# Kernel tuning notes

Hardware: AMD Instinct MI355X
Metric: run time of the kernel (lower is better)

## Reference

```python
import jax, jax.numpy as jnp
import numpy as np

D_MODEL = 512; DEPTH = 4; HEADS = 8; BUCKET = 256; N_HASHES = 4
INPUT_DIM = 32; SEQ = 2 * BUCKET; BATCH = 16; DH = D_MODEL // HEADS
N_BUCKETS = SEQ // BUCKET  # 2 (seq_len is forced to 2*bucket_size by pos_encoding)
SELF_ATTN_VALUE = -5e4  # TOKEN_SELF_ATTN_VALUE in reformer_pytorch


def layer_norm(x, g, b, eps=1e-5):
    m = jnp.mean(x, -1, keepdims=True)
    v = jnp.mean((x - m) ** 2, -1, keepdims=True)
    return (x - m) / jnp.sqrt(v + eps) * g + b


def look_one_back(x):
    # each chunk also attends to the previous chunk (circularly)
    prev = jnp.concatenate([x[:, -1:], x[:, :-1]], axis=1)
    return jnp.concatenate([x, prev], axis=2)


def lsh_attention(qk, v, rot):
    # qk, v: (B*H, T, DH); rot: (DH, N_HASHES, N_BUCKETS//2). Shared-QK LSH attention.
    B, T, d = qk.shape
    rotated = jnp.einsum('btf,fhi->bhti', qk, rot)                  # (B, nh, T, nb/2)
    rotated = jnp.concatenate([rotated, -rotated], axis=-1)        # (B, nh, T, nb)
    buckets = jnp.argmax(rotated, axis=-1)                          # (B, nh, T)
    offsets = (jnp.arange(N_HASHES) * N_BUCKETS)[None, :, None]
    buckets = (buckets + offsets).reshape(B, N_HASHES * T)
    ticker = jnp.arange(N_HASHES * T) % T
    bkt = T * buckets + ticker[None, :]                             # unique sort keys
    sticker = jnp.argsort(bkt, axis=-1)
    undo = jnp.argsort(sticker, axis=-1)
    st = sticker % T
    sqk = jnp.take_along_axis(qk, st[..., None], axis=1)            # (B, nh*T, d)
    sv = jnp.take_along_axis(v, st[..., None], axis=1)
    nch = N_HASHES * N_BUCKETS
    bq_t = st.reshape(B, nch, -1)
    bqk = sqk.reshape(B, nch, -1, d)
    bv = sv.reshape(B, nch, -1, d)
    bq = bqk
    bk = bqk / jnp.maximum(jnp.linalg.norm(bqk, axis=-1, keepdims=True), 1e-12)
    bk = look_one_back(bk)
    bv = look_one_back(bv)
    bkv_t = look_one_back(bq_t[..., None])[..., 0]
    dots = jnp.einsum('bcie,bcje->bcij', bq, bk) * (d ** -0.5)      # (B, nch, c, 2c)
    neg = -jnp.finfo(dots.dtype).max
    dots = jnp.where(bq_t[:, :, :, None] < bkv_t[:, :, None, :], neg, dots)   # causal
    dots = jnp.where(bq_t[:, :, :, None] == bkv_t[:, :, None, :], SELF_ATTN_VALUE, dots)  # de-prioritize self
    lse = jax.scipy.special.logsumexp(dots, axis=-1, keepdims=True)
    p = jnp.exp(dots - lse)
    bo = jnp.einsum('bcij,bcje->bcie', p, bv)
    so = bo.reshape(B, N_HASHES * T, d)
    sl = lse.reshape(B, N_HASHES * T)
    o = jnp.take_along_axis(so, undo[..., None], axis=1).reshape(B, N_HASHES, T, d)
    lg = jnp.take_along_axis(sl, undo, axis=1).reshape(B, N_HASHES, T, 1)
    w = jnp.exp(lg - jax.scipy.special.logsumexp(lg, axis=1, keepdims=True))  # combine hash rounds
    return jnp.sum(o * w, axis=1)


def lsh_self_attn(x, wqk, wv, wo, wo_b, rot):
    b, t, dm = x.shape
    split = lambda z: z.reshape(b, t, HEADS, DH).transpose(0, 2, 1, 3).reshape(b * HEADS, t, DH)
    o = lsh_attention(split(x @ wqk), split(x @ wv), rot)
    o = o.reshape(b, HEADS, t, DH).transpose(0, 2, 1, 3).reshape(b, t, dm)
    return o @ wo + wo_b


def setup_inputs() -> dict:
    key = jax.random.key(0)
    ks = jax.random.split(key, 12)
    f = lambda k, shape: jax.random.normal(k, shape, jnp.float32) * 0.02
    D, DEP, FF = D_MODEL, DEPTH, 4 * D_MODEL
    return {
        'x': jax.random.normal(ks[0], (BATCH, SEQ, INPUT_DIM), jnp.float32),
        'emb_w': f(ks[1], (INPUT_DIM, D)), 'emb_b': jnp.zeros((D,), jnp.float32),
        'pos': f(ks[2], (1, SEQ, D)),
        'ln1_g': jnp.ones((DEP, D), jnp.float32), 'ln1_b': jnp.zeros((DEP, D), jnp.float32),
        'wqk': f(ks[3], (DEP, D, D)), 'wv': f(ks[4], (DEP, D, D)),
        'wo': f(ks[5], (DEP, D, D)), 'wo_b': jnp.zeros((DEP, D), jnp.float32),
        'ln2_g': jnp.ones((DEP, D), jnp.float32), 'ln2_b': jnp.zeros((DEP, D), jnp.float32),
        'ff_w1': f(ks[6], (DEP, D, FF)), 'ff_b1': jnp.zeros((DEP, FF), jnp.float32),
        'ff_w2': f(ks[7], (DEP, FF, D)), 'ff_b2': jnp.zeros((DEP, D), jnp.float32),
        'rot': jax.random.normal(ks[8], (DEP, DH, N_HASHES, N_BUCKETS // 2), jnp.float32),
        'lnf_g': jnp.ones((D,), jnp.float32), 'lnf_b': jnp.zeros((D,), jnp.float32),
        'hw1': f(ks[9], (D, D // 2)), 'hb1': jnp.zeros((D // 2,), jnp.float32),
        'hln_g': jnp.ones((D // 2,), jnp.float32), 'hln_b': jnp.zeros((D // 2,), jnp.float32),
        'hw2': f(ks[10], (D // 2, 1)), 'hb2': jnp.zeros((1,), jnp.float32),
    }


def reference(x, emb_w, emb_b, pos, ln1_g, ln1_b, wqk, wv, wo, wo_b, ln2_g, ln2_b,
              ff_w1, ff_b1, ff_w2, ff_b2, rot, lnf_g, lnf_b, hw1, hb1, hln_g, hln_b, hw2, hb2):
    h = x @ emb_w + emb_b + pos
    # reversible residual stack (forward math): x1 += attn(norm(x2)); x2 += ff(norm(x1))
    x1 = h
    x2 = h
    for i in range(DEPTH):
        x1 = x1 + lsh_self_attn(layer_norm(x2, ln1_g[i], ln1_b[i]), wqk[i], wv[i], wo[i], wo_b[i], rot[i])
        hn = layer_norm(x1, ln2_g[i], ln2_b[i])
        x2 = x2 + jax.nn.gelu(hn @ ff_w1[i] + ff_b1[i], approximate=False) @ ff_w2[i] + ff_b2[i]
    h = 0.5 * (x1 + x2)
    h = layer_norm(h, lnf_g, lnf_b)[:, -1, :]
    h = jax.nn.relu(layer_norm(h @ hw1 + hb1, hln_g, hln_b))
    return h @ hw2 + hb2
```

## Files before the change

kernel.cpp:

```cpp
#include <hip/hip_runtime.h>
#include <hip/hip_fp16.h>
#include <cfloat>
#include <cstdint>

#define BB      16
#define TT      512
#define DD      512
#define HH      8
#define DHH     64
#define FFD     2048
#define BHH     128
#define NHASH   4
#define NCHUNK  8
#define CHUNKSZ 256
#define NLAYER  4

typedef unsigned short u16;
typedef unsigned int   u32;
typedef __attribute__((ext_vector_type(8))) short bfrag;
typedef __attribute__((ext_vector_type(4))) float f4x;
typedef __attribute__((ext_vector_type(16))) float f16x;

union FragU { u32 u[4]; uint4 v4; bfrag f; };

__device__ __forceinline__ unsigned pk_bf16(float a, float b) {
    union { float f; unsigned u; } x, y;
    x.f = a; y.f = b;
    unsigned lo = ((x.u + 0x7FFFu + ((x.u >> 16) & 1u)) >> 16) & 0xFFFFu;
    unsigned hi = (y.u + 0x7FFFu + ((y.u >> 16) & 1u)) & 0xFFFF0000u;
    return lo | hi;
}
__device__ __forceinline__ unsigned cvt_pk(float a, float b) {
    unsigned r;
    asm("v_cvt_pk_bf16_f32 %0, %1, %2" : "=v"(r) : "v"(a), "v"(b));
    return r;
}
__device__ __forceinline__ unsigned pkrtz(float a, float b) {
    unsigned r;
    asm("v_cvt_pkrtz_f16_f32 %0, %1, %2" : "=v"(r) : "v"(a), "v"(b));
    return r;
}
__device__ __forceinline__ u16 bf16_1(float a) {
    union { float f; unsigned u; } x; x.f = a;
    return (u16)((x.u + 0x7FFFu + ((x.u >> 16) & 1u)) >> 16);
}
__device__ __forceinline__ float b2f(u16 h) {
    union { unsigned u; float f; } x; x.u = ((unsigned)h) << 16; return x.f;
}

__device__ __forceinline__ void gload16(const u16* g, u16* l) {
    __builtin_amdgcn_global_load_lds(
        (const __attribute__((address_space(1))) u32*)g,
        (__attribute__((address_space(3))) u32*)l, 16, 0, 0);
}

__global__ __launch_bounds__(256)
void embed_kernel(const float* __restrict__ x, const float* __restrict__ ew,
                  const float* __restrict__ eb, const float* __restrict__ pos,
                  float* __restrict__ x1, float* __restrict__ x2)
{
    const int row = blockIdx.x;
    const int t = row & (TT - 1);
    __shared__ float xr[32];
    if (threadIdx.x < 32) xr[threadIdx.x] = x[row * 32 + threadIdx.x];
    __syncthreads();
    for (int d = threadIdx.x; d < DD; d += 256) {
        float s = eb[d] + pos[t * DD + d];
        #pragma unroll
        for (int k = 0; k < 32; ++k) s = fmaf(xr[k], ew[k * DD + d], s);
        x1[(size_t)row * DD + d] = s;
        x2[(size_t)row * DD + d] = s;
    }
}

__global__ __launch_bounds__(256)
void ln_kernel(const float* __restrict__ in, const float* __restrict__ g,
               const float* __restrict__ bta, float* __restrict__ out,
               u16* __restrict__ outh)
{
    const int row = blockIdx.x * 4 + (threadIdx.x >> 6);
    const int lane = threadIdx.x & 63;
    const float* r = in + (size_t)row * DD;
    float vals[8];
    float s = 0.0f;
    #pragma unroll
    for (int i = 0; i < 8; ++i) { vals[i] = r[i * 64 + lane]; s += vals[i]; }
    #pragma unroll
    for (int o = 1; o < 64; o <<= 1) s += __shfl_xor(s, o);
    const float mean = s * (1.0f / 512.0f);
    float vs = 0.0f;
    #pragma unroll
    for (int i = 0; i < 8; ++i) { float d = vals[i] - mean; vs += d * d; }
    #pragma unroll
    for (int o = 1; o < 64; o <<= 1) vs += __shfl_xor(vs, o);
    const float rstd = rsqrtf(vs * (1.0f / 512.0f) + 1e-5f);
    u16* hrow = outh + (size_t)row * DD;
    #pragma unroll
    for (int i = 0; i < 8; ++i) {
        const int d = i * 64 + lane;
        const float y = (vals[i] - mean) * rstd * g[d] + bta[d];
        if (out != nullptr) out[(size_t)row * DD + d] = y;
        hrow[d] = bf16_1(y);
    }
}

__global__ __launch_bounds__(256)
void prep_weights(const float* __restrict__ wqk, const float* __restrict__ wv,
                  const float* __restrict__ wo, const float* __restrict__ ffw1,
                  const float* __restrict__ ffw2,
                  u16* __restrict__ wqkT, u16* __restrict__ wvT,
                  u16* __restrict__ woT, u16* __restrict__ w1T,
                  u16* __restrict__ w2T)
{
    const int id = blockIdx.x;
    const float* in; u16* outp; int K, N, kt, nt;
    if (id < 3072) {
        const int fam = id >> 10;
        const int r = id & 1023;
        const int L = r >> 8, t = r & 255;
        K = 512; N = 512;
        const size_t off = (size_t)L * 512 * 512;
        in   = (fam == 0 ? wqk  : fam == 1 ? wv  : wo ) + off;
        outp = (fam == 0 ? wqkT : fam == 1 ? wvT : woT) + off;
        kt = (t & 15) << 5; nt = (t >> 4) << 5;
    } else if (id < 7168) {
        const int r = id - 3072;
        const int L = r >> 10, t = r & 1023;
        K = 512; N = 2048;
        in = ffw1 + (size_t)L * 512 * 2048;
        outp = w1T + (size_t)L * 2048 * 512;
        kt = (t & 15) << 5; nt = (t >> 4) << 5;
    } else {
        const int r = id - 7168;
        const int L = r >> 10, t = r & 1023;
        K = 2048; N = 512;
        in = ffw2 + (size_t)L * 2048 * 512;
        outp = w2T + (size_t)L * 512 * 2048;
        kt = (t & 63) << 5; nt = (t >> 6) << 5;
    }
    __shared__ float tile[32][33];
    const int rr = threadIdx.x >> 3, c4 = (threadIdx.x & 7) * 4;
    const float4 v4 = *(const float4*)(in + (size_t)(kt + rr) * N + nt + c4);
    tile[rr][c4 + 0] = v4.x; tile[rr][c4 + 1] = v4.y;
    tile[rr][c4 + 2] = v4.z; tile[rr][c4 + 3] = v4.w;
    __syncthreads();
    uint2 p;
    p.x = pk_bf16(tile[c4 + 0][rr], tile[c4 + 1][rr]);
    p.y = pk_bf16(tile[c4 + 2][rr], tile[c4 + 3][rr]);
    *(uint2*)(outp + (size_t)(nt + rr) * K + kt + c4) = p;
}

__global__ __launch_bounds__(256)
void wrot_kernel(const float* __restrict__ wqk, const float* __restrict__ rot,
                 float* __restrict__ wrotAll)
{
    const int hh = blockIdx.x, L = blockIdx.y;
    const int head = hh >> 2, h = hh & 3;
    __shared__ float rc[64];
    if (threadIdx.x < 64)
        rc[threadIdx.x] = rot[((size_t)L * 64 + threadIdx.x) * 4 + h];
    __syncthreads();
    for (int f = threadIdx.x; f < 512; f += 256) {
        const float* wrow = wqk + (size_t)L * 512 * 512 + (size_t)f * 512 + head * 64;
        float s = 0.0f;
        #pragma unroll
        for (int d = 0; d < 64; d += 4) {
            const float4 w4 = *(const float4*)(wrow + d);
            s += w4.x * rc[d] + w4.y * rc[d + 1] + w4.z * rc[d + 2] + w4.w * rc[d + 3];
        }
        wrotAll[((size_t)L * 512 + f) * 32 + hh] = s;
    }
}

__global__ __launch_bounds__(256)
void rot_gemm(const float* __restrict__ A, const float* __restrict__ Wr,
              float* __restrict__ C)
{
    __shared__ float As[64][36];
    __shared__ float Ws[32][36];
    const int m0 = blockIdx.x * 64;
    const int r = threadIdx.x >> 2, cg = threadIdx.x & 3;
    float acc[8] = {};
    for (int f0 = 0; f0 < 512; f0 += 32) {
        __syncthreads();
        {
            const int lr = threadIdx.x >> 2, lc = (threadIdx.x & 3) * 8;
            const float* ap = A + (size_t)(m0 + lr) * 512 + f0 + lc;
            *(float4*)&As[lr][lc]     = ((const float4*)ap)[0];
            *(float4*)&As[lr][lc + 4] = ((const float4*)ap)[1];
            const int wr = threadIdx.x >> 3, wc = (threadIdx.x & 7) * 4;
            *(float4*)&Ws[wr][wc] = *(const float4*)(Wr + (size_t)(f0 + wr) * 32 + wc);
        }
        __syncthreads();
        #pragma unroll
        for (int kk = 0; kk < 32; ++kk) {
            const float a = As[r][kk];
            #pragma unroll
            for (int c = 0; c < 8; ++c)
                acc[c] = fmaf(a, Ws[kk][cg * 8 + c], acc[c]);
        }
    }
    float* crow = C + (size_t)(m0 + r) * 32 + cg * 8;
    *(float4*)crow       = make_float4(acc[0], acc[1], acc[2], acc[3]);
    *(float4*)(crow + 4) = make_float4(acc[4], acc[5], acc[6], acc[7]);
}

__device__ __forceinline__ float gelu1(float v) {
    return 0.5f * v * (1.0f + erff(v * 0.70710678118654752440f));
}
__device__ __forceinline__ int swz_row(int r, int BK) {
    return (BK == 32) ? ((r & 3) ^ ((r >> 2) & 3)) : (r & 7);
}

template<int BM, int BN, int BK, bool GELU, bool ADD, bool BIAS, bool OUTBF, bool QKL>
__global__ __launch_bounds__(256)
void gemm_bf16(const u16* __restrict__ A, const u16* __restrict__ WT,
               const float* __restrict__ bias, const float* __restrict__ addsrc,
               float* __restrict__ Cf, u16* __restrict__ Cb,
               int M, int N, int K)
{
    constexpr int NCH = BK / 8;
    constexpr int CPA = BM * NCH / 256;
    constexpr int CPB = BN * NCH / 256;
    constexpr int MR = BM / 32, NR = BN / 32, KR = BK / 32;
    __shared__ __align__(16) u16 Abuf[2][BM * BK];
    __shared__ __align__(16) u16 Bbuf[2][BN * BK];
    const int tid = threadIdx.x;
    const int m0 = blockIdx.x * BM, n0 = blockIdx.y * BN;

    const u16* aSrc[CPA]; const u16* bSrc[CPB];
    #pragma unroll
    for (int i = 0; i < CPA; ++i) {
        const int s = tid + i * 256, row = s / NCH, ch = s % NCH;
        aSrc[i] = A + (size_t)(m0 + row) * K + (ch ^ swz_row(row, BK)) * 8;
    }
    #pragma unroll
    for (int i = 0; i < CPB; ++i) {
        const int s = tid + i * 256, row = s / NCH, ch = s % NCH;
        bSrc[i] = WT + (size_t)(n0 + row) * K + (ch ^ swz_row(row, BK)) * 8;
    }

    auto STAGE = [&](int bufi, int koff) {
        #pragma unroll
        for (int i = 0; i < CPA; ++i)
            gload16(aSrc[i] + koff, &Abuf[bufi][(tid + i * 256) * 8]);
        #pragma unroll
        for (int i = 0; i < CPB; ++i)
            gload16(bSrc[i] + koff, &Bbuf[bufi][(tid + i * 256) * 8]);
    };

    const int l = tid & 63, wv_ = tid >> 6;
    const int wm = (wv_ >> 1) * (BM / 2);
    const int wn = (wv_ & 1) * (BN / 2);
    const int fr = l & 15, fc = l >> 4;

    f4x acc[MR][NR] = {};
    const int nK = K / BK;
    STAGE(0, 0);
    for (int ks = 0; ks < nK; ++ks) {
        __syncthreads();
        if (ks + 1 < nK) STAGE((ks + 1) & 1, (ks + 1) * BK);
        const u16* Ab = Abuf[ks & 1];
        const u16* Bb = Bbuf[ks & 1];
        FragU af[MR][KR], bf_[NR][KR];
        #pragma unroll
        for (int i = 0; i < MR; ++i)
            #pragma unroll
            for (int u = 0; u < KR; ++u) {
                const int r = wm + i * 16 + fr;
                af[i][u].v4 = *(const uint4*)((const char*)Ab +
                    (size_t)r * (2 * BK) + (((u * 4 + fc) ^ swz_row(r, BK)) << 4));
            }
        #pragma unroll
        for (int j = 0; j < NR; ++j)
            #pragma unroll
            for (int u = 0; u < KR; ++u) {
                const int r = wn + j * 16 + fr;
                bf_[j][u].v4 = *(const uint4*)((const char*)Bb +
                    (size_t)r * (2 * BK) + (((u * 4 + fc) ^ swz_row(r, BK)) << 4));
            }
        #pragma unroll
        for (int u = 0; u < KR; ++u)
            #pragma unroll
            for (int i = 0; i < MR; ++i)
                #pragma unroll
                for (int j = 0; j < NR; ++j)
                    acc[i][j] = __builtin_amdgcn_mfma_f32_16x16x32_bf16(
                        af[i][u].f, bf_[j][u].f, acc[i][j], 0, 0, 0);
    }

    #pragma unroll
    for (int i = 0; i < MR; ++i) {
        #pragma unroll
        for (int q = 0; q < 4; ++q) {
            const int row = m0 + wm + i * 16 + fc * 4 + q;
            #pragma unroll
            for (int j = 0; j < NR; ++j) {
                const int col = n0 + wn + j * 16 + fr;
                float vx = acc[i][j][q];
                if constexpr (BIAS) vx += bias[col];
                if constexpr (GELU) vx = gelu1(vx);
                if constexpr (ADD) vx += addsrc[(size_t)row * N + col];
                if constexpr (QKL) {
                    const int bq = row >> 9, tq = row & 511;
                    const int hq = col >> 6, dq = col & 63;
                    Cb[(((size_t)(bq * 8 + hq) * 512) + tq) * 64 + dq] = bf16_1(vx);
                } else if constexpr (OUTBF) {
                    Cb[(size_t)row * N + col] = bf16_1(vx);
                } else {
                    Cf[(size_t)row * N + col] = vx;
                }
            }
        }
    }
}

__global__ __launch_bounds__(256)
void knorm_kernel(const u16* __restrict__ qkh, u16* __restrict__ qkn,
                  float* __restrict__ qnrm)
{
    const int g = blockIdx.x * 16 + (threadIdx.x >> 4);
    const int li = threadIdx.x & 15;
    const uint2 raw = *(const uint2*)(qkh + (size_t)g * 64 + li * 4);
    const float v0 = b2f((u16)(raw.x & 0xffff)), v1 = b2f((u16)(raw.x >> 16));
    const float v2 = b2f((u16)(raw.y & 0xffff)), v3 = b2f((u16)(raw.y >> 16));
    float ss = v0 * v0 + v1 * v1 + v2 * v2 + v3 * v3;
    ss += __shfl_xor(ss, 1); ss += __shfl_xor(ss, 2);
    ss += __shfl_xor(ss, 4); ss += __shfl_xor(ss, 8);
    const float qn = sqrtf(ss);
    const float rv = 1.0f / fmaxf(qn, 1e-12f);
    uint2 o;
    o.x = cvt_pk(v0 * rv, v1 * rv);
    o.y = cvt_pk(v2 * rv, v3 * rv);
    *(uint2*)(qkn + (size_t)g * 64 + li * 4) = o;
    if (li == 0) qnrm[g] = qn;
}

__global__ __launch_bounds__(512)
void bucket_sort_kernel(const float* __restrict__ rotated, int* __restrict__ st)
{
    const int h = blockIdx.x, bh = blockIdx.y;
    const int b = bh >> 3, head = bh & 7;
    const int t = threadIdx.x;
    __shared__ int zcnt[8];
    const float r = rotated[((size_t)(b * TT + t)) * 32 + head * 4 + h];
    const int bit = (r < 0.0f) ? 1 : 0;
    const int wid = t >> 6, lane = t & 63;
    const unsigned long long zm = __ballot(bit == 0);
    if (lane == 0) zcnt[wid] = __popcll(zm);
    __syncthreads();
    int zoff = 0, Z = 0;
    #pragma unroll
    for (int w = 0; w < 8; ++w) { const int cn = zcnt[w]; if (w < wid) zoff += cn; Z += cn; }
    const int zpre = __popcll(zm & ((1ull << lane) - 1ull));
    const int dst = (bit == 0) ? (zoff + zpre)
                               : (Z + (wid * 64 - zoff) + (lane - zpre));
    st[((size_t)bh * NHASH + h) * TT + dst] = t;
}

__global__ __launch_bounds__(512, 4)
void lsh_attn_mfma(const u16* __restrict__ qkn, const u16* __restrict__ v,
                   const float* __restrict__ qnrm, const int* __restrict__ st,
                   __half* __restrict__ o_hash, float* __restrict__ lse_hash)
{
    const int cc = blockIdx.x, bh = blockIdx.y;
    const int b = bh >> 3, head = bh & 7;
    const int h = cc >> 1, c = cc & 1;
    const int pcc = (cc + 7) & 7;
    const int hp = pcc >> 1, cp = pcc & 1;
    const int tid = threadIdx.x;
    const int w = tid >> 6;
    const int lane = tid & 63;
    const int l31 = lane & 31;
    const int hi = lane >> 5;
    const int* stb = st + (size_t)bh * (NHASH * TT);
    const size_t vbase = ((size_t)b * TT) * DD + head * DHH;
    const u16* qknb = qkn + (size_t)bh * TT * DHH;

    __shared__ __align__(16) u16 Kbf[64 * 64];
    __shared__ __align__(16) u16 VTbf[64 * 64];
    __shared__ __align__(16) int ktl[64];

    const int q_t = stb[h * TT + c * CHUNKSZ + w * 32 + l31];
    const float qn = qnrm[(size_t)bh * TT + q_t];
    const float mnat = qn * 0.125f;
    const float aC = qn * 0.1803368801111137f;
    uint4 QF4[4];
    {
        const u16* qrow = qknb + (size_t)q_t * DHH;
        #pragma unroll
        for (int ds = 0; ds < 4; ++ds)
            QF4[ds] = *(const uint4*)(qrow + ds * 16 + hi * 8);
    }

    f16x acc[2] = {};
    float lacc = 0.f;
    const int k8 = tid >> 3;
    const int c8 = tid & 7;

    auto gather = [&](int t8, uint4& kc, uint4& vc, int& ktc) {
        const int kj = t8 * 64 + k8;
        const int k_t = (kj < CHUNKSZ) ? stb[h * TT + c * CHUNKSZ + kj]
                                       : stb[hp * TT + cp * CHUNKSZ + (kj - CHUNKSZ)];
        ktc = k_t;
        kc = *(const uint4*)(qknb + (size_t)k_t * DHH + c8 * 8);
        vc = *(const uint4*)(v + vbase + (size_t)k_t * DD + c8 * 8);
    };

    uint4 kc, vc; int ktc;
    gather(0, kc, vc, ktc);

    for (int kt8 = 0; kt8 < 8; ++kt8) {
        __syncthreads();
        *(uint4*)((char*)Kbf + ((k8 * 128 + c8 * 16) ^ ((k8 & 7) << 4))) = kc;
        {
            const unsigned vu[4] = {vc.x, vc.y, vc.z, vc.w};
            #pragma unroll
            for (int i = 0; i < 8; ++i) {
                const int d = c8 * 8 + i;
                const u16 hv = (u16)((i & 1) ? (vu[i >> 1] >> 16) : (vu[i >> 1] & 0xffff));
                *(u16*)((char*)VTbf + ((d * 128 + k8 * 2) ^ (i << 4))) = hv;
            }
        }
        if (c8 == 0) ktl[k8] = ktc;
        __syncthreads();

        const int t8n = (kt8 < 7) ? kt8 + 1 : 0;
        gather(t8n, kc, vc, ktc);

        #pragma unroll
        for (int kt = 0; kt < 2; ++kt) {
            int4 kt4[4];
            #pragma unroll
            for (int j = 0; j < 4; ++j)
                kt4[j] = *(const int4*)&ktl[kt * 32 + 8 * j + 4 * hi];
            const int* ktvp = (const int*)kt4;
            FragU KA[4];
            #pragma unroll
            for (int ds = 0; ds < 4; ++ds) {
                const int row = kt * 32 + l31;
                KA[ds].v4 = *(const uint4*)((const char*)Kbf +
                    ((row * 128 + ds * 32 + hi * 16) ^ ((row & 7) << 4)));
            }
            FragU VA[2][2];
            #pragma unroll
            for (int dt = 0; dt < 2; ++dt)
                #pragma unroll
                for (int u = 0; u < 2; ++u) {
                    const int row = dt * 32 + l31;
                    const int ks = kt * 2 + u;
                    VA[dt][u].v4 = *(const uint4*)((const char*)VTbf +
                        ((row * 128 + ks * 32 + hi * 16) ^ ((row & 7) << 4)));
                }
            f16x s = {0.f,0.f,0.f,0.f,0.f,0.f,0.f,0.f,
                      0.f,0.f,0.f,0.f,0.f,0.f,0.f,0.f};
            #pragma unroll
            for (int ds = 0; ds < 4; ++ds) {
                FragU qf; qf.v4 = QF4[ds];
                s = __builtin_amdgcn_mfma_f32_32x32x16_bf16(KA[ds].f, qf.f, s, 0, 0, 0);
            }
            float pv[16];
            #pragma unroll
            for (int i = 0; i < 16; ++i) {
                const float e = exp2f(fmaf(s[i], aC, -aC));
                const float p = (q_t > ktvp[i]) ? e : 0.0f;
                pv[i] = p;
                lacc += p;
            }
            unsigned P2[8];
            #pragma unroll
            for (int g = 0; g < 4; ++g) {
                P2[2*g]   = cvt_pk(pv[4*g],   pv[4*g+1]);
                P2[2*g+1] = cvt_pk(pv[4*g+2], pv[4*g+3]);
            }
            #pragma unroll
            for (int u = 0; u < 2; ++u) {
                unsigned a0 = P2[4*u + 0], b0 = P2[4*u + 2];
                unsigned a1 = P2[4*u + 1], b1 = P2[4*u + 3];
                asm("v_permlane32_swap_b32 %0, %1" : "+v"(a0), "+v"(b0));
                asm("v_permlane32_swap_b32 %0, %1" : "+v"(a1), "+v"(b1));
                FragU bfv;
                bfv.u[0] = a0; bfv.u[1] = a1; bfv.u[2] = b0; bfv.u[3] = b1;
                #pragma unroll
                for (int dt = 0; dt < 2; ++dt)
                    acc[dt] = __builtin_amdgcn_mfma_f32_32x32x16_bf16(
                        VA[dt][u].f, bfv.f, acc[dt], 0, 0, 0);
            }
        }
    }

    const float lt = lacc + __shfl_xor(lacc, 32);
    const float invl = (lt > 0.f) ? 1.0f / lt : 0.0f;
    if (hi == 0) {
        const float lse = (lt > 0.f) ? (mnat + logf(lt)) : -5.0e4f;
        lse_hash[(size_t)(bh * NHASH + h) * TT + q_t] = lse;
    }
    unsigned wa[8], wb[8];
    #pragma unroll
    for (int m = 0; m < 8; ++m) {
        wa[m] = pkrtz(acc[0][2*m] * invl, acc[0][2*m+1] * invl);
        wb[m] = pkrtz(acc[1][2*m] * invl, acc[1][2*m+1] * invl);
    }
    #pragma unroll
    for (int m = 0; m < 8; ++m)
        asm("v_permlane32_swap_b32 %0, %1" : "+v"(wa[m]), "+v"(wb[m]));
    __half* orow = o_hash + ((size_t)(bh * NHASH + h) * TT + q_t) * DHH + hi * 32;
    if (lt > 0.f) {
        #pragma unroll
        for (int g = 0; g < 4; ++g) {
            uint4 o;
            o.x = wa[2*g]; o.y = wa[2*g+1];
            o.z = wb[2*g]; o.w = wb[2*g+1];
            ((uint4*)orow)[g] = o;
        }
    } else {
        const u16* vr = v + vbase + (size_t)q_t * DD + hi * 32;
        #pragma unroll
        for (int g = 0; g < 4; ++g) {
            uint4 o;
            o.x = pkrtz(b2f(vr[8*g+0]), b2f(vr[8*g+1]));
            o.y = pkrtz(b2f(vr[8*g+2]), b2f(vr[8*g+3]));
            o.z = pkrtz(b2f(vr[8*g+4]), b2f(vr[8*g+5]));
            o.w = pkrtz(b2f(vr[8*g+6]), b2f(vr[8*g+7]));
            ((uint4*)orow)[g] = o;
        }
    }
}

__global__ __launch_bounds__(256)
void combine_kernel(const __half* __restrict__ o_hash, const float* __restrict__ lse_hash,
                    u16* __restrict__ am)
{
    const int idx = blockIdx.x * 4 + (threadIdx.x >> 6);
    const int lane = threadIdx.x & 63;
    const int bh = idx >> 9, t = idx & 511;
    const int b = bh >> 3, head = bh & 7;
    const float ls0 = lse_hash[(size_t)(bh * NHASH + 0) * TT + t];
    const float ls1 = lse_hash[(size_t)(bh * NHASH + 1) * TT + t];
    const float ls2 = lse_hash[(size_t)(bh * NHASH + 2) * TT + t];
    const float ls3 = lse_hash[(size_t)(bh * NHASH + 3) * TT + t];
    const float M = fmaxf(fmaxf(ls0, ls1), fmaxf(ls2, ls3));
    const float e0 = __expf(ls0 - M), e1 = __expf(ls1 - M);
    const float e2 = __expf(ls2 - M), e3 = __expf(ls3 - M);
    const float inv = 1.0f / (e0 + e1 + e2 + e3);
    const float o =
        (e0 * __half2float(o_hash[((size_t)((bh * NHASH + 0) * TT + t)) * DHH + lane]) +
         e1 * __half2float(o_hash[((size_t)((bh * NHASH + 1) * TT + t)) * DHH + lane]) +
         e2 * __half2float(o_hash[((size_t)((bh * NHASH + 2) * TT + t)) * DHH + lane]) +
         e3 * __half2float(o_hash[((size_t)((bh * NHASH + 3) * TT + t)) * DHH + lane])) * inv;
    am[((size_t)(b * TT + t)) * DD + head * DHH + lane] = bf16_1(o);
}

__device__ __forceinline__ float block_sum256(float v, volatile float* red)
{
    const int lane = threadIdx.x & 63, wid = threadIdx.x >> 6;
    #pragma unroll
    for (int o = 1; o < 64; o <<= 1) v += __shfl_xor(v, o);
    __syncthreads();
    if (lane == 0) red[wid] = v;
    __syncthreads();
    return red[0] + red[1] + red[2] + red[3];
}

__global__ __launch_bounds__(256)
void head_kernel(const float* __restrict__ x1, const float* __restrict__ x2,
                 const float* __restrict__ lnfg, const float* __restrict__ lnfb,
                 const float* __restrict__ hw1, const float* __restrict__ hb1,
                 const float* __restrict__ hlng, const float* __restrict__ hlnb,
                 const float* __restrict__ hw2, const float* __restrict__ hb2,
                 float* __restrict__ out)
{
    __shared__ float nrow[512];
    __shared__ float red[4];
    const int b = blockIdx.x, tid = threadIdx.x;
    const size_t roff = ((size_t)b * TT + (TT - 1)) * DD;
    const float v0 = 0.5f * (x1[roff + tid] + x2[roff + tid]);
    const float v1 = 0.5f * (x1[roff + 256 + tid] + x2[roff + 256 + tid]);
    const float mean = block_sum256(v0 + v1, red) * (1.0f / 512.0f);
    const float d0 = v0 - mean, d1 = v1 - mean;
    const float var = block_sum256(d0 * d0 + d1 * d1, red) * (1.0f / 512.0f);
    const float rstd = rsqrtf(var + 1e-5f);
    nrow[tid]       = d0 * rstd * lnfg[tid] + lnfb[tid];
    nrow[tid + 256] = d1 * rstd * lnfg[tid + 256] + lnfb[tid + 256];
    __syncthreads();
    float a = hb1[tid];
    for (int k = 0; k < 512; ++k) a = fmaf(nrow[k], hw1[(size_t)k * 256 + tid], a);
    const float m2 = block_sum256(a, red) * (1.0f / 256.0f);
    const float dd = a - m2;
    const float var2 = block_sum256(dd * dd, red) * (1.0f / 256.0f);
    float y = dd * rsqrtf(var2 + 1e-5f) * hlng[tid] + hlnb[tid];
    y = fmaxf(y, 0.0f);
    const float osum = block_sum256(y * hw2[tid], red);
    if (tid == 0) out[b] = osum + hb2[0];
}

extern "C" void kernel_launch(void* const* d_in, const int* in_sizes, int n_in,
                              void* d_out, int out_size, void* d_ws, size_t ws_size,
                              hipStream_t stream)
{
    (void)in_sizes; (void)n_in; (void)out_size; (void)ws_size;
    const float* x    = (const float*)d_in[0];
    const float* embw = (const float*)d_in[1];
    const float* embb = (const float*)d_in[2];
    const float* pos  = (const float*)d_in[3];
    const float* ln1g = (const float*)d_in[4];
    const float* ln1b = (const float*)d_in[5];
    const float* wqk  = (const float*)d_in[6];
    const float* wv   = (const float*)d_in[7];
    const float* wo   = (const float*)d_in[8];
    const float* wob  = (const float*)d_in[9];
    const float* ln2g = (const float*)d_in[10];
    const float* ln2b = (const float*)d_in[11];
    const float* ffw1 = (const float*)d_in[12];
    const float* ffb1 = (const float*)d_in[13];
    const float* ffw2 = (const float*)d_in[14];
    const float* ffb2 = (const float*)d_in[15];
    const float* rot  = (const float*)d_in[16];
    const float* lnfg = (const float*)d_in[17];
    const float* lnfb = (const float*)d_in[18];
    const float* hw1  = (const float*)d_in[19];
    const float* hb1  = (const float*)d_in[20];
    const float* hlng = (const float*)d_in[21];
    const float* hlnb = (const float*)d_in[22];
    const float* hw2  = (const float*)d_in[23];
    const float* hb2  = (const float*)d_in[24];
    float* out = (float*)d_out;

    const size_t SZ_BTD = (size_t)BB * TT * DD;
    const size_t SZ_OH  = (size_t)BHH * NHASH * TT * DHH;

    char* p = (char*)d_ws;
    float* x1b = (float*)p;  p += SZ_BTD * 4;
    float* x2b = (float*)p;  p += SZ_BTD * 4;
    float* xnb = (float*)p;  p += SZ_BTD * 4;
    u16*   vbh = (u16*)p;    p += SZ_BTD * 2;
    u16*   xnbh = (u16*)p;   p += SZ_BTD * 2;
    u16*   qkh  = (u16*)p;   p += SZ_BTD * 2;
    u16*   qknb = (u16*)p;   p += (size_t)BHH * TT * DHH * 2;
    float* qnrm = (float*)p; p += (size_t)BHH * TT * 4;
    float* rotated = (float*)p; p += (size_t)BB * TT * 32 * 4;
    __half* ohash = (__half*)p;
    u16*    ffmid = (u16*)p;
    p += SZ_OH * 2;
    float* lseb  = (float*)p; p += (size_t)BHH * NHASH * TT * 4;
    int*   stb   = (int*)p;   p += (size_t)BHH * NHASH * TT * 4;
    u16* wqkT = (u16*)p; p += (size_t)NLAYER * DD * DD * 2;
    u16* wvT  = (u16*)p; p += (size_t)NLAYER * DD * DD * 2;
    u16* woT  = (u16*)p; p += (size_t)NLAYER * DD * DD * 2;
    u16* w1T  = (u16*)p; p += (size_t)NLAYER * DD * FFD * 2;
    u16* w2T  = (u16*)p; p += (size_t)NLAYER * FFD * DD * 2;
    float* wrotAll = (float*)p; p += (size_t)NLAYER * DD * 32 * 4;
    u16* amb = (u16*)xnb;

    prep_weights<<<11264, 256, 0, stream>>>(wqk, wv, wo, ffw1, ffw2,
                                            wqkT, wvT, woT, w1T, w2T);
    wrot_kernel<<<dim3(32, NLAYER), 256, 0, stream>>>(wqk, rot, wrotAll);

    embed_kernel<<<BB * TT, 256, 0, stream>>>(x, embw, embb, pos, x1b, x2b);

    for (int L = 0; L < NLAYER; ++L) {
        const size_t w512 = (size_t)L * DD * DD;
        const size_t wff  = (size_t)L * DD * FFD;

        ln_kernel<<<2048, 256, 0, stream>>>(x2b, ln1g + L * DD, ln1b + L * DD, xnb, xnbh);
        rot_gemm<<<128, 256, 0, stream>>>(xnb, wrotAll + (size_t)L * DD * 32, rotated);
        gemm_bf16<64, 64, 64, false, false, false, true, true><<<dim3(128, 8), 256, 0, stream>>>(
            xnbh, wqkT + w512, nullptr, nullptr, nullptr, qkh, BB * TT, DD, DD);
        gemm_bf16<64, 64, 64, false, false, false, true, false><<<dim3(128, 8), 256, 0, stream>>>(
            xnbh, wvT + w512, nullptr, nullptr, nullptr, vbh, BB * TT, DD, DD);
        bucket_sort_kernel<<<dim3(NHASH, BHH), 512, 0, stream>>>(rotated, stb);
        knorm_kernel<<<4096, 256, 0, stream>>>(qkh, qknb, qnrm);
        lsh_attn_mfma<<<dim3(NCHUNK, BHH), 512, 0, stream>>>(
            qknb, vbh, qnrm, stb, ohash, lseb);
        combine_kernel<<<16384, 256, 0, stream>>>(ohash, lseb, amb);
        gemm_bf16<64, 64, 64, false, true, true, false, false><<<dim3(128, 8), 256, 0, stream>>>(
            amb, woT + w512, wob + L * DD, x1b, x1b, nullptr, BB * TT, DD, DD);

        ln_kernel<<<2048, 256, 0, stream>>>(x1b, ln2g + L * DD, ln2b + L * DD, nullptr, xnbh);
        gemm_bf16<128, 128, 32, true, false, true, true, false><<<dim3(64, 16), 256, 0, stream>>>(
            xnbh, w1T + wff, ffb1 + L * FFD, nullptr, nullptr, ffmid, BB * TT, FFD, DD);
        gemm_bf16<64, 64, 64, false, true, true, false, false><<<dim3(128, 8), 256, 0, stream>>>(
            ffmid, w2T + wff, ffb2 + L * DD, x2b, x2b, nullptr, BB * TT, DD, FFD);
    }

    head_kernel<<<16, 256, 0, stream>>>(x1b, x2b, lnfg, lnfb, hw1, hb1,
                                        hlng, hlnb, hw2, hb2, out);
}
```

Measured before the change: 947.9 us.

## Fuse QK and V projections into one GEMM; double-buffer LSH attention tiles

The separate QK and V projection GEMMs become a single GEMM over a concatenated 1024-wide transposed weight, using 128x128 tiles. Column blocks below 512 write the head-major QK layout and the rest write the V buffer, which is passed through the float output pointer. Separately, the LSH attention kernel now double-buffers its K/V shared-memory tiles, prefetching the next tile while computing and dropping one barrier per iteration. It also changes the V-transpose swizzle to a bit-reversed slot scheme to cut LDS bank conflicts. This doubles LDS use in the attention kernel, which may reduce occupancy.

```diff
diff --git a/kernel.cpp b/kernel.cpp
--- a/kernel.cpp
+++ b/kernel.cpp
@@ -108,9 +108,8 @@
 void prep_weights(const float* __restrict__ wqk, const float* __restrict__ wv,
                   const float* __restrict__ wo, const float* __restrict__ ffw1,
                   const float* __restrict__ ffw2,
-                  u16* __restrict__ wqkT, u16* __restrict__ wvT,
-                  u16* __restrict__ woT, u16* __restrict__ w1T,
-                  u16* __restrict__ w2T)
+                  u16* __restrict__ wqkvT, u16* __restrict__ woT,
+                  u16* __restrict__ w1T, u16* __restrict__ w2T)
 {
     const int id = blockIdx.x;
     const float* in; u16* outp; int K, N, kt, nt;
@@ -120,8 +119,9 @@
         const int L = r >> 8, t = r & 255;
         K = 512; N = 512;
         const size_t off = (size_t)L * 512 * 512;
-        in   = (fam == 0 ? wqk  : fam == 1 ? wv  : wo ) + off;
-        outp = (fam == 0 ? wqkT : fam == 1 ? wvT : woT) + off;
+        in = (fam == 0 ? wqk : fam == 1 ? wv : wo) + off;
+        outp = (fam == 2) ? (woT + off)
+                          : (wqkvT + (size_t)L * 1024 * 512 + (fam == 1 ? (size_t)512 * 512 : 0));
         kt = (t & 15) << 5; nt = (t >> 4) << 5;
     } else if (id < 7168) {
         const int r = id - 3072;
@@ -212,7 +212,7 @@
     return (BK == 32) ? ((r & 3) ^ ((r >> 2) & 3)) : (r & 7);
 }
 
-template<int BM, int BN, int BK, bool GELU, bool ADD, bool BIAS, bool OUTBF, bool QKL>
+template<int BM, int BN, int BK, bool GELU, bool ADD, bool BIAS, bool OUTBF, bool QKV>
 __global__ __launch_bounds__(256)
 void gemm_bf16(const u16* __restrict__ A, const u16* __restrict__ WT,
                const float* __restrict__ bias, const float* __restrict__ addsrc,
@@ -301,10 +301,14 @@
                 if constexpr (BIAS) vx += bias[col];
                 if constexpr (GELU) vx = gelu1(vx);
                 if constexpr (ADD) vx += addsrc[(size_t)row * N + col];
-                if constexpr (QKL) {
-                    const int bq = row >> 9, tq = row & 511;
-                    const int hq = col >> 6, dq = col & 63;
-                    Cb[(((size_t)(bq * 8 + hq) * 512) + tq) * 64 + dq] = bf16_1(vx);
+                if constexpr (QKV) {
+                    if (n0 < 512) {
+                        const int bq = row >> 9, tq = row & 511;
+                        const int hq = col >> 6, dq = col & 63;
+                        Cb[(((size_t)(bq * 8 + hq) * 512) + tq) * 64 + dq] = bf16_1(vx);
+                    } else {
+                        ((u16*)Cf)[(size_t)row * 512 + (col - 512)] = bf16_1(vx);
+                    }
                 } else if constexpr (OUTBF) {
                     Cb[(size_t)row * N + col] = bf16_1(vx);
                 } else {
@@ -377,9 +381,9 @@
     const size_t vbase = ((size_t)b * TT) * DD + head * DHH;
     const u16* qknb = qkn + (size_t)bh * TT * DHH;
 
-    __shared__ __align__(16) u16 Kbf[64 * 64];
-    __shared__ __align__(16) u16 VTbf[64 * 64];
-    __shared__ __align__(16) int ktl[64];
+    __shared__ __align__(16) u16 Kbf[2][64 * 64];
+    __shared__ __align__(16) u16 VTbf[2][64 * 64];
+    __shared__ __align__(16) int ktl[2][64];
 
     const int q_t = stb[h * TT + c * CHUNKSZ + w * 32 + l31];
     const float qn = qnrm[(size_t)bh * TT + q_t];
@@ -397,6 +401,10 @@
     float lacc = 0.f;
     const int k8 = tid >> 3;
     const int c8 = tid & 7;
+    const int brc = ((c8 & 1) << 2) | (c8 & 2) | ((c8 & 4) >> 2);
+    const int wSlot = ((k8 >> 3) + brc) & 7;
+    const int g2 = l31 >> 3;
+    const int brg = ((g2 & 1) << 2) | (g2 & 2);
 
     auto gather = [&](int t8, uint4& kc, uint4& vc, int& ktc) {
         const int kj = t8 * 64 + k8;
@@ -406,40 +414,42 @@
         kc = *(const uint4*)(qknb + (size_t)k_t * DHH + c8 * 8);
         vc = *(const uint4*)(v + vbase + (size_t)k_t * DD + c8 * 8);
     };
+    auto writeTile = [&](int bi, const uint4& kc, const uint4& vc, int ktc) {
+        *(uint4*)((char*)Kbf[bi] + ((k8 * 128 + c8 * 16) ^ ((k8 & 7) << 4))) = kc;
+        const unsigned vu[4] = {vc.x, vc.y, vc.z, vc.w};
+        #pragma unroll
+        for (int i = 0; i < 8; ++i) {
+            const int d = c8 * 8 + i;
+            const u16 hv = (u16)((i & 1) ? (vu[i >> 1] >> 16) : (vu[i >> 1] & 0xffff));
+            *(u16*)((char*)VTbf[bi] + d * 128 + wSlot * 16 + (k8 & 7) * 2) = hv;
+        }
+        if (c8 == 0) ktl[bi][k8] = ktc;
+    };
 
     uint4 kc, vc; int ktc;
     gather(0, kc, vc, ktc);
+    writeTile(0, kc, vc, ktc);
+    __syncthreads();
 
     for (int kt8 = 0; kt8 < 8; ++kt8) {
-        __syncthreads();
-        *(uint4*)((char*)Kbf + ((k8 * 128 + c8 * 16) ^ ((k8 & 7) << 4))) = kc;
-        {
-            const unsigned vu[4] = {vc.x, vc.y, vc.z, vc.w};
-            #pragma unroll
-            for (int i = 0; i < 8; ++i) {
-                const int d = c8 * 8 + i;
-                const u16 hv = (u16)((i & 1) ? (vu[i >> 1] >> 16) : (vu[i >> 1] & 0xffff));
-                *(u16*)((char*)VTbf + ((d * 128 + k8 * 2) ^ (i << 4))) = hv;
-            }
-        }
-        if (c8 == 0) ktl[k8] = ktc;
-        __syncthreads();
-
-        const int t8n = (kt8 < 7) ? kt8 + 1 : 0;
-        gather(t8n, kc, vc, ktc);
+        const int cur = kt8 & 1;
+        if (kt8 < 7) gather(kt8 + 1, kc, vc, ktc);
+        const u16* Kb = Kbf[cur];
+        const u16* Vb = VTbf[cur];
+        const int* kl = ktl[cur];
 
         #pragma unroll
         for (int kt = 0; kt < 2; ++kt) {
             int4 kt4[4];
             #pragma unroll
             for (int j = 0; j < 4; ++j)
-                kt4[j] = *(const int4*)&ktl[kt * 32 + 8 * j + 4 * hi];
+                kt4[j] = *(const int4*)&kl[kt * 32 + 8 * j + 4 * hi];
             const int* ktvp = (const int*)kt4;
             FragU KA[4];
             #pragma unroll
             for (int ds = 0; ds < 4; ++ds) {
                 const int row = kt * 32 + l31;
-                KA[ds].v4 = *(const uint4*)((const char*)Kbf +
+                KA[ds].v4 = *(const uint4*)((const char*)Kb +
                     ((row * 128 + ds * 32 + hi * 16) ^ ((row & 7) << 4)));
             }
             FragU VA[2][2];
@@ -448,9 +458,10 @@
                 #pragma unroll
                 for (int u = 0; u < 2; ++u) {
                     const int row = dt * 32 + l31;
-                    const int ks = kt * 2 + u;
-                    VA[dt][u].v4 = *(const uint4*)((const char*)VTbf +
-                        ((row * 128 + ks * 32 + hi * 16) ^ ((row & 7) << 4)));
+                    const int cr = (kt * 2 + u) * 2 + hi;
+                    const int slot = (cr + brg + dt) & 7;
+                    VA[dt][u].v4 = *(const uint4*)((const char*)Vb +
+                        row * 128 + slot * 16);
                 }
             f16x s = {0.f,0.f,0.f,0.f,0.f,0.f,0.f,0.f,
                       0.f,0.f,0.f,0.f,0.f,0.f,0.f,0.f};
@@ -486,6 +497,11 @@
                     acc[dt] = __builtin_amdgcn_mfma_f32_32x32x16_bf16(
                         VA[dt][u].f, bfv.f, acc[dt], 0, 0, 0);
             }
+        }
+
+        if (kt8 < 7) {
+            writeTile(cur ^ 1, kc, vc, ktc);
+            __syncthreads();
         }
     }
 
@@ -644,16 +660,15 @@
     p += SZ_OH * 2;
     float* lseb  = (float*)p; p += (size_t)BHH * NHASH * TT * 4;
     int*   stb   = (int*)p;   p += (size_t)BHH * NHASH * TT * 4;
-    u16* wqkT = (u16*)p; p += (size_t)NLAYER * DD * DD * 2;
-    u16* wvT  = (u16*)p; p += (size_t)NLAYER * DD * DD * 2;
-    u16* woT  = (u16*)p; p += (size_t)NLAYER * DD * DD * 2;
-    u16* w1T  = (u16*)p; p += (size_t)NLAYER * DD * FFD * 2;
-    u16* w2T  = (u16*)p; p += (size_t)NLAYER * FFD * DD * 2;
+    u16* wqkvT = (u16*)p; p += (size_t)NLAYER * 1024 * 512 * 2;
+    u16* woT   = (u16*)p; p += (size_t)NLAYER * DD * DD * 2;
+    u16* w1T   = (u16*)p; p += (size_t)NLAYER * DD * FFD * 2;
+    u16* w2T   = (u16*)p; p += (size_t)NLAYER * FFD * DD * 2;
     float* wrotAll = (float*)p; p += (size_t)NLAYER * DD * 32 * 4;
     u16* amb = (u16*)xnb;
 
     prep_weights<<<11264, 256, 0, stream>>>(wqk, wv, wo, ffw1, ffw2,
-                                            wqkT, wvT, woT, w1T, w2T);
+                                            wqkvT, woT, w1T, w2T);
     wrot_kernel<<<dim3(32, NLAYER), 256, 0, stream>>>(wqk, rot, wrotAll);
 
     embed_kernel<<<BB * TT, 256, 0, stream>>>(x, embw, embb, pos, x1b, x2b);
@@ -664,10 +679,9 @@
 
         ln_kernel<<<2048, 256, 0, stream>>>(x2b, ln1g + L * DD, ln1b + L * DD, xnb, xnbh);
         rot_gemm<<<128, 256, 0, stream>>>(xnb, wrotAll + (size_t)L * DD * 32, rotated);
-        gemm_bf16<64, 64, 64, false, false, false, true, true><<<dim3(128, 8), 256, 0, stream>>>(
-            xnbh, wqkT + w512, nullptr, nullptr, nullptr, qkh, BB * TT, DD, DD);
-        gemm_bf16<64, 64, 64, false, false, false, true, false><<<dim3(128, 8), 256, 0, stream>>>(
-            xnbh, wvT + w512, nullptr, nullptr, nullptr, vbh, BB * TT, DD, DD);
+        gemm_bf16<128, 128, 32, false, false, false, false, true><<<dim3(64, 8), 256, 0, stream>>>(
+            xnbh, wqkvT + (size_t)L * 1024 * 512, nullptr, nullptr,
+            (float*)vbh, qkh, BB * TT, 1024, DD);
         bucket_sort_kernel<<<dim3(NHASH, BHH), 512, 0, stream>>>(rotated, stb);
         knorm_kernel<<<4096, 256, 0, stream>>>(qkh, qknb, qnrm);
         lsh_attn_mfma<<<dim3(NCHUNK, BHH), 512, 0, stream>>>(
```

Result: faster. 923.9 us (-2.5%).
